# Performance work log

Hardware: AMD Instinct MI355X
Metric: run time of the kernel (lower is better)

## Reference

```python
import jax, jax.numpy as jnp
import numpy as np

HIDDEN = 2048
HEADS = 32
HEAD_DIM = HIDDEN // HEADS  # 64
MAX_POS = 512
TABLE = 2 * MAX_POS - 1  # 1023


def setup_inputs() -> dict:
    key = jax.random.key(0)
    k = jax.random.split(key, 6)
    B, S = 16, 512
    return {
        "hidden_states": jax.random.normal(k[0], (B, S, HIDDEN), dtype=jnp.float32),
        "wq": jax.random.normal(k[1], (HIDDEN, HIDDEN), dtype=jnp.float32) * 0.02,
        "wk": jax.random.normal(k[2], (HIDDEN, HIDDEN), dtype=jnp.float32) * 0.02,
        "wv": jax.random.normal(k[3], (HIDDEN, HIDDEN), dtype=jnp.float32) * 0.02,
        "wo": jax.random.normal(k[4], (HIDDEN, HIDDEN), dtype=jnp.float32) * 0.02,
        "rel_pos": jax.random.normal(k[5], (TABLE, HEAD_DIM), dtype=jnp.float32),
    }


def _rel_bias(rel_pos, seq_len):
    pos = jnp.arange(seq_len)
    rel = pos[None, :] - pos[:, None] + (MAX_POS - 1)  # [S, S]
    rel = jnp.clip(rel, 0, TABLE - 1)
    return rel_pos[rel].mean(axis=-1)  # [S, S]


def reference(hidden_states, wq, wk, wv, wo, rel_pos):
    B, S, _ = hidden_states.shape
    scale = jnp.sqrt(jnp.float32(HEAD_DIM))
    # nn.Linear(x) = x @ W.T
    q = (hidden_states @ wq.T).reshape(B, S, HEADS, HEAD_DIM).transpose(0, 2, 1, 3)
    k = (hidden_states @ wk.T).reshape(B, S, HEADS, HEAD_DIM).transpose(0, 2, 1, 3)
    v = (hidden_states @ wv.T).reshape(B, S, HEADS, HEAD_DIM).transpose(0, 2, 1, 3)
    scores = jnp.einsum("bhqd,bhkd->bhqk", q, k) / scale
    scores = scores + _rel_bias(rel_pos, S)[None, None]  # seq_len <= 512 path
    attn = jax.nn.softmax(scores, axis=-1)
    ctx = jnp.einsum("bhqk,bhkd->bhqd", attn, v)
    ctx = ctx.transpose(0, 2, 1, 3).reshape(B, S, HIDDEN)
    return ctx @ wo.T
```

## Files before the change

### kernel.cpp

```cpp
#include <hip/hip_runtime.h>

typedef __attribute__((ext_vector_type(8))) short bf16x8;
typedef __attribute__((ext_vector_type(4))) float f32x4;
typedef const __attribute__((address_space(3))) unsigned short* lds_cp;

#define DEVI __device__ __forceinline__

template <int N> struct IC { static constexpr int v = N; };

DEVI unsigned short f2bf(float f) {
  union { float f; unsigned u; } v; v.f = f;
  unsigned r = v.u + 0x7FFFu + ((v.u >> 16) & 1u);
  return (unsigned short)(r >> 16);
}

DEVI void gload16(const void* g, void* l) {
  __builtin_amdgcn_global_load_lds(
      (const __attribute__((address_space(1))) unsigned int*)g,
      (__attribute__((address_space(3))) unsigned int*)l, 16, 0, 0);
}

template <int OFF>
DEVI bf16x8 lreadT(lds_cp p) {
  bf16x8 r;
  asm volatile("ds_read_b128 %0, %1 offset:%2" : "=v"(r) : "v"(p), "i"(OFF));
  return r;
}

template <int OFF>
DEVI void read_af(lds_cp a0, lds_cp a1, bf16x8 (&f)[4][2]) {
  f[0][0] = lreadT<OFF + 0>(a0);    f[0][1] = lreadT<OFF + 0>(a1);
  f[1][0] = lreadT<OFF + 2048>(a0); f[1][1] = lreadT<OFF + 2048>(a1);
  f[2][0] = lreadT<OFF + 4096>(a0); f[2][1] = lreadT<OFF + 4096>(a1);
  f[3][0] = lreadT<OFF + 6144>(a0); f[3][1] = lreadT<OFF + 6144>(a1);
}
template <int OFF>
DEVI void read_bq(lds_cp b0, lds_cp b1, bf16x8 (&f)[2][2]) {
  f[0][0] = lreadT<OFF + 0>(b0);    f[0][1] = lreadT<OFF + 0>(b1);
  f[1][0] = lreadT<OFF + 2048>(b0); f[1][1] = lreadT<OFF + 2048>(b1);
}

#define MFMA16(a, b, c) __builtin_amdgcn_mfma_f32_16x16x32_bf16(a, b, c, 0, 0, 0)
#define LGKM(n) asm volatile("s_waitcnt lgkmcnt(" #n ")")
#define SBAR() __builtin_amdgcn_sched_barrier(0)

__global__ void prep_kernel(const float* __restrict__ x,
                            const float* __restrict__ wq,
                            const float* __restrict__ wk,
                            const float* __restrict__ wv,
                            const float* __restrict__ wo,
                            const float* __restrict__ rel,
                            unsigned short* __restrict__ xb,
                            unsigned short* __restrict__ wqb,
                            float* __restrict__ bias1) {
  const int blk = blockIdx.x;
  if (blk < 16384) {
    const int i = blk * 256 + threadIdx.x;
    float4 v = ((const float4*)x)[i];
    ushort4 o;
    o.x = f2bf(v.x); o.y = f2bf(v.y); o.z = f2bf(v.z); o.w = f2bf(v.w);
    ((ushort4*)xb)[i] = o;
  } else if (blk < 32768) {
    const int i = (blk - 16384) * 256 + threadIdx.x;
    const int w = i >> 20, l = i & 1048575;
    const float* s = (w == 0) ? wq : (w == 1) ? wk : (w == 2) ? wv : wo;
    float4 v = ((const float4*)s)[l];
    ushort4 o;
    o.x = f2bf(v.x); o.y = f2bf(v.y); o.z = f2bf(v.z); o.w = f2bf(v.w);
    ((ushort4*)wqb)[i] = o;
  } else {
    const int t = (blk - 32768) * 256 + threadIdx.x;
    if (t < 1023) {
      const float* r = rel + t * 64;
      float s = 0.f;
#pragma unroll
      for (int d = 0; d < 64; ++d) s += r[d];
      bias1[t] = s * (1.44269504f / 64.0f);
    }
  }
}

template <int MODE, int NT>
__global__ __launch_bounds__(512, 2) void gemm256(
    const unsigned short* __restrict__ A, const unsigned short* __restrict__ B,
    void* __restrict__ Cout, void* __restrict__ Cout2, void* __restrict__ Cout3) {
  __shared__ unsigned short As[2][16384];
  __shared__ unsigned short Bs[2][16384];

  const int tid = threadIdx.x;
  const int logical = (blockIdx.x & 7) * (4 * NT) + (blockIdx.x >> 3);
  const int nt = logical % NT, mt = logical / NT;
  const int m0 = mt * 256, n0 = nt * 256;
  const int lane = tid & 63, wid = tid >> 6;
  const int wr = wid >> 2, wc = wid & 3;
  const int g = lane >> 4, c = lane & 15;

  const int srow = tid >> 3, sj = (tid & 7) ^ (srow & 7);
  const unsigned short* pA0[2];
  const unsigned short* pB0[2];
  unsigned short* lA0[2];
  unsigned short* lB0[2];
#pragma unroll
  for (int ch = 0; ch < 2; ++ch) {
    const int row = ch * 64 + srow;
    pA0[ch] = A + (size_t)(m0 + row) * 2048u + sj * 8;
    pB0[ch] = B + (size_t)(n0 + row) * 2048u + sj * 8;
    const int slot = ch * 512 + tid;
    lA0[ch] = &As[0][slot * 8];
    lB0[ch] = &Bs[0][slot * 8];
  }

  const int rA = wr * 128 + c;
  const int rB = wc * 64 + c;
  lds_cp aA0 = (lds_cp)&As[0][rA * 64 + (((0 + g) ^ (rA & 7)) * 8)];
  lds_cp aA1 = (lds_cp)&As[0][rA * 64 + (((4 + g) ^ (rA & 7)) * 8)];
  lds_cp aB0 = (lds_cp)&Bs[0][rB * 64 + (((0 + g) ^ (rB & 7)) * 8)];
  lds_cp aB1 = (lds_cp)&Bs[0][rB * 64 + (((4 + g) ^ (rB & 7)) * 8)];

  f32x4 acc[8][4];
#pragma unroll
  for (int i = 0; i < 8; ++i)
#pragma unroll
    for (int j = 0; j < 4; ++j) acc[i][j] = (f32x4){0.f, 0.f, 0.f, 0.f};

  bf16x8 afl[4][2], afh[4][2], bq0[2][2], bq1[2][2];

#pragma unroll
  for (int ch = 0; ch < 2; ++ch) {
    gload16(pA0[ch], lA0[ch]);
    gload16(pA0[ch] + 262144, lA0[ch] + 8192);
    gload16(pB0[ch], lB0[ch]);
    gload16(pB0[ch] + 262144, lB0[ch] + 8192);
  }
#pragma unroll
  for (int ch = 0; ch < 2; ++ch) {
    gload16(pA0[ch] + 64, lA0[ch] + 16384);
    gload16(pA0[ch] + 262144 + 64, lA0[ch] + 8192 + 16384);
  }
  asm volatile("s_waitcnt vmcnt(4)" ::: "memory");
  SBAR();
  __builtin_amdgcn_s_barrier();

  auto ktile = [&](auto B_, auto SB_, auto SA_, auto LB_, auto LA_, int kt) {
    constexpr int BOFF = decltype(B_)::v;
    constexpr int SB = decltype(SB_)::v;
    constexpr int SA = decltype(SA_)::v;
    constexpr int LB = decltype(LB_)::v;
    constexpr int LA = decltype(LA_)::v;

    read_bq<BOFF>(aB0, aB1, bq0);
    read_af<BOFF>(aA0, aA1, afl);
    read_bq<BOFF + 4096>(aB0, aB1, bq1);
    read_af<BOFF + 8192>(aA0, aA1, afh);
    if (kt + 1 < 32) {
      gload16(pB0[0] + SB, lB0[0] + LB);
      gload16(pB0[1] + SB, lB0[1] + LB);
      gload16(pB0[0] + 262144 + SB, lB0[0] + 8192 + LB);
      gload16(pB0[1] + 262144 + SB, lB0[1] + 8192 + LB);
    }

    LGKM(12);
    SBAR();
    __builtin_amdgcn_s_setprio(1);
#pragma unroll
    for (int kk = 0; kk < 2; ++kk)
#pragma unroll
      for (int mi = 0; mi < 4; ++mi)
#pragma unroll
        for (int ni = 0; ni < 2; ++ni)
          acc[mi][ni] = MFMA16(afl[mi][kk], bq0[ni][kk], acc[mi][ni]);
    __builtin_amdgcn_s_setprio(0);

    LGKM(8);
    SBAR();
    __builtin_amdgcn_s_setprio(1);
#pragma unroll
    for (int kk = 0; kk < 2; ++kk)
#pragma unroll
      for (int mi = 0; mi < 4; ++mi)
#pragma unroll
        for (int ni = 0; ni < 2; ++ni)
          acc[mi][ni + 2] = MFMA16(afl[mi][kk], bq1[ni][kk], acc[mi][ni + 2]);
    __builtin_amdgcn_s_setprio(0);

    LGKM(0);
    SBAR();
    __builtin_amdgcn_s_barrier();
    if (kt + 2 < 32) {
      gload16(pA0[0] + SA, lA0[0] + LA);
      gload16(pA0[1] + SA, lA0[1] + LA);
      gload16(pA0[0] + 262144 + SA, lA0[0] + 8192 + LA);
      gload16(pA0[1] + 262144 + SA, lA0[1] + 8192 + LA);
    }

    __builtin_amdgcn_s_setprio(1);
#pragma unroll
    for (int kk = 0; kk < 2; ++kk)
#pragma unroll
      for (int mi = 0; mi < 4; ++mi)
#pragma unroll
        for (int ni = 0; ni < 2; ++ni)
          acc[mi + 4][ni] = MFMA16(afh[mi][kk], bq0[ni][kk], acc[mi + 4][ni]);
#pragma unroll
    for (int kk = 0; kk < 2; ++kk)
#pragma unroll
      for (int mi = 0; mi < 4; ++mi)
#pragma unroll
        for (int ni = 0; ni < 2; ++ni)
          acc[mi + 4][ni + 2] = MFMA16(afh[mi][kk], bq1[ni][kk], acc[mi + 4][ni + 2]);
    __builtin_amdgcn_s_setprio(0);

    if (kt < 30) {
      asm volatile("s_waitcnt vmcnt(4)" ::: "memory");
    } else {
      asm volatile("s_waitcnt vmcnt(0)" ::: "memory");
    }
    SBAR();
    __builtin_amdgcn_s_barrier();
  };

  for (int t2 = 0; t2 < 16; ++t2) {
    ktile(IC<0>{}, IC<64>{}, IC<128>{}, IC<16384>{}, IC<0>{}, 2 * t2);
    ktile(IC<32768>{}, IC<128>{}, IC<192>{}, IC<0>{}, IC<16384>{}, 2 * t2 + 1);
#pragma unroll
    for (int ch = 0; ch < 2; ++ch) { pA0[ch] += 128; pB0[ch] += 128; }
  }

  const int rbase = m0 + wr * 128 + g * 4;
  const int cbase = n0 + wc * 64 + c;
  if (MODE == 0) {
    float* O = (float*)Cout;
#pragma unroll
    for (int mi = 0; mi < 8; ++mi)
#pragma unroll
      for (int ni = 0; ni < 4; ++ni)
#pragma unroll
        for (int rr = 0; rr < 4; ++rr)
          O[(size_t)(rbase + mi * 16 + rr) * 2048u + (cbase + ni * 16)] =
              acc[mi][ni][rr];
  } else {
    const int qsel = cbase >> 11;
    if (qsel < 2) {
      unsigned short* O = (unsigned short*)(qsel == 0 ? Cout : Cout2);
#pragma unroll
      for (int mi = 0; mi < 8; ++mi)
#pragma unroll
        for (int ni = 0; ni < 4; ++ni)
#pragma unroll
          for (int rr = 0; rr < 4; ++rr)
            O[(size_t)(rbase + mi * 16 + rr) * 2048u +
              ((cbase + ni * 16) & 2047)] = f2bf(acc[mi][ni][rr]);
    } else {
      unsigned short* O = (unsigned short*)Cout3;
#pragma unroll
      for (int mi = 0; mi < 8; ++mi)
#pragma unroll
        for (int ni = 0; ni < 4; ++ni) {
          const int row = rbase + mi * 16;
          const int col = (cbase + ni * 16) & 2047;
          const int bq_ = row >> 9, s = row & 511;
          const int hh = col >> 6, dd = col & 63;
          ushort4 o;
          o.x = f2bf(acc[mi][ni][0]);
          o.y = f2bf(acc[mi][ni][1]);
          o.z = f2bf(acc[mi][ni][2]);
          o.w = f2bf(acc[mi][ni][3]);
          *(ushort4*)(O + ((size_t)((bq_ * 32 + hh) * 64 + dd) << 9) + s) = o;
        }
    }
  }
}

__global__ __launch_bounds__(256, 3) void attn_kernel(
    const unsigned short* __restrict__ Q, const unsigned short* __restrict__ K,
    const unsigned short* __restrict__ VT, const float* __restrict__ bias1d,
    unsigned short* __restrict__ CTX) {
  __shared__ unsigned short Ksh[2][4096];
  __shared__ unsigned short Vsh[2][4096];
  __shared__ unsigned short Pb[4][2048];
  __shared__ float bl[1024];

  const int tid = threadIdx.x;
  const int wave = tid >> 6;
  const int lane = tid & 63;
  const int g = lane >> 4, c = lane & 15;

  const int logical = (blockIdx.x & 7) * 256 + (blockIdx.x >> 3);
  const int qc = logical & 3;
  const int bh = logical >> 2;
  const int b = bh >> 5, h = bh & 31;
  const int qrow0 = qc * 128 + wave * 32;

  for (int i = tid; i < 1023; i += 256) bl[i] = bias1d[i];

  bf16x8 aq[2][2];
  {
    const unsigned short* qb =
        Q + (size_t)(b * 512 + qrow0 + c) * 2048u + h * 64 + g * 8;
#pragma unroll
    for (int mi = 0; mi < 2; ++mi)
#pragma unroll
      for (int kk = 0; kk < 2; ++kk)
        aq[mi][kk] = *(const bf16x8*)(qb + mi * 16 * 2048 + kk * 32);
  }

  const unsigned short* kgb = K + (size_t)(b * 512) * 2048u + h * 64;
  const unsigned short* vgb = VT + (size_t)(bh * 64) * 512u;

  auto stage = [&](int buf, int kt) {
#pragma unroll
    for (int half = 0; half < 2; ++half) {
      const int slot = half * 256 + wave * 64 + lane;
      const int row = slot >> 3;
      const int j = (slot & 7) ^ (row & 7);
      gload16(kgb + (size_t)(kt * 64 + row) * 2048u + j * 8,
              &Ksh[buf][slot * 8]);
      gload16(vgb + (size_t)row * 512u + kt * 64 + j * 8, &Vsh[buf][slot * 8]);
    }
  };

  f32x4 o[2][4];
#pragma unroll
  for (int mi = 0; mi < 2; ++mi)
#pragma unroll
    for (int di = 0; di < 4; ++di) o[mi][di] = (f32x4){0.f, 0.f, 0.f, 0.f};
  float lreg[2][4];
#pragma unroll
  for (int mi = 0; mi < 2; ++mi)
#pragma unroll
    for (int rr = 0; rr < 4; ++rr) lreg[mi][rr] = 0.f;

  stage(0, 0);
  __syncthreads();

  const float SSCALE = 0.125f * 1.44269504f;

  for (int kt = 0; kt < 8; ++kt) {
    const int buf = kt & 1;
    if (kt < 7) stage(buf ^ 1, kt + 1);

    f32x4 s[2][4];
#pragma unroll
    for (int ni = 0; ni < 4; ++ni) {
      const unsigned short* kr = &Ksh[buf][(ni * 16 + c) * 64];
      bf16x8 bk0 = *(const bf16x8*)(kr + ((0 + g) ^ (c & 7)) * 8);
      bf16x8 bk1 = *(const bf16x8*)(kr + ((4 + g) ^ (c & 7)) * 8);
#pragma unroll
      for (int mi = 0; mi < 2; ++mi) {
        f32x4 z = (f32x4){0.f, 0.f, 0.f, 0.f};
        z = MFMA16(aq[mi][0], bk0, z);
        z = MFMA16(aq[mi][1], bk1, z);
        s[mi][ni] = z;
      }
    }

    unsigned short* pw = &Pb[wave][0];
#pragma unroll
    for (int mi = 0; mi < 2; ++mi)
#pragma unroll
      for (int rr = 0; rr < 4; ++rr) {
        const int prow = mi * 16 + g * 4 + rr;
        const int off0 = kt * 64 + c - (qrow0 + prow) + 511;
        float e0 = __builtin_amdgcn_exp2f(s[mi][0][rr] * SSCALE + bl[off0]);
        float e1 = __builtin_amdgcn_exp2f(s[mi][1][rr] * SSCALE + bl[off0 + 16]);
        float e2 = __builtin_amdgcn_exp2f(s[mi][2][rr] * SSCALE + bl[off0 + 32]);
        float e3 = __builtin_amdgcn_exp2f(s[mi][3][rr] * SSCALE + bl[off0 + 48]);
        lreg[mi][rr] += (e0 + e1) + (e2 + e3);
        const int rx = prow * 64, sw = (c >> 3) ^ (prow & 7), cl = c & 7;
        pw[rx + ((0 ^ sw) * 8 | cl)] = f2bf(e0);
        pw[rx + ((2 ^ sw) * 8 | cl)] = f2bf(e1);
        pw[rx + ((4 ^ sw) * 8 | cl)] = f2bf(e2);
        pw[rx + ((6 ^ sw) * 8 | cl)] = f2bf(e3);
      }

#pragma unroll
    for (int kk = 0; kk < 2; ++kk) {
      bf16x8 pa0 =
          *(const bf16x8*)(pw + (0 + c) * 64 + ((kk * 4 + g) ^ (c & 7)) * 8);
      bf16x8 pa1 =
          *(const bf16x8*)(pw + (16 + c) * 64 + ((kk * 4 + g) ^ (c & 7)) * 8);
#pragma unroll
      for (int di = 0; di < 4; ++di) {
        bf16x8 vb = *(const bf16x8*)(&Vsh[buf][(di * 16 + c) * 64 +
                                               ((kk * 4 + g) ^ (c & 7)) * 8]);
        o[0][di] = MFMA16(pa0, vb, o[0][di]);
        o[1][di] = MFMA16(pa1, vb, o[1][di]);
      }
    }
    __syncthreads();
  }

#pragma unroll
  for (int mi = 0; mi < 2; ++mi)
#pragma unroll
    for (int rr = 0; rr < 4; ++rr) {
      float l = lreg[mi][rr];
      l += __shfl_xor(l, 1);
      l += __shfl_xor(l, 2);
      l += __shfl_xor(l, 4);
      l += __shfl_xor(l, 8);
      const float rl = __builtin_amdgcn_rcpf(l);
      unsigned short* ob =
          CTX + (size_t)(b * 512 + qrow0 + mi * 16 + g * 4 + rr) * 2048u +
          h * 64 + c;
#pragma unroll
      for (int di = 0; di < 4; ++di) ob[di * 16] = f2bf(o[mi][di][rr] * rl);
    }
}

extern "C" void kernel_launch(void* const* d_in, const int* in_sizes, int n_in,
                              void* d_out, int out_size, void* d_ws,
                              size_t ws_size, hipStream_t stream) {
  const float* x = (const float*)d_in[0];
  const float* wq = (const float*)d_in[1];
  const float* wk = (const float*)d_in[2];
  const float* wv = (const float*)d_in[3];
  const float* wo = (const float*)d_in[4];
  const float* rel = (const float*)d_in[5];

  char* ws = (char*)d_ws;
  unsigned short* xb = (unsigned short*)(ws);
  unsigned short* wqb = (unsigned short*)(ws + 33554432);
  unsigned short* wob = wqb + 3 * 4194304;
  unsigned short* qb = (unsigned short*)(ws + 67108864);
  unsigned short* kb = qb + 16777216;
  unsigned short* vt = kb + 16777216;
  float* bias1 = (float*)(ws + 167772160);
  unsigned short* ctx = xb;

  prep_kernel<<<32772, 256, 0, stream>>>(x, wq, wk, wv, wo, rel, xb, wqb,
                                         bias1);

  gemm256<3, 24><<<768, 512, 0, stream>>>(xb, wqb, qb, kb, vt);

  attn_kernel<<<2048, 256, 0, stream>>>(qb, kb, vt, bias1, ctx);

  gemm256<0, 8><<<256, 512, 0, stream>>>(ctx, wob, (float*)d_out, nullptr,
                                         nullptr);
}
```

Baseline: 334.0 us.

## Load K/V fragments directly from global in attention, drop LDS staging

Removes the double-buffered LDS staging of K and V tiles in the attention kernel. Each wave now reads its MFMA B-operands straight from global memory (relying on L1/L2 for reuse across the four waves) and no longer synchronises per tile. Freeing LDS allows the launch bound to rise to four blocks per CU, and s_setprio wraps the MFMA sections. The trade is redundant global/cache traffic across waves and exposed load latency, since there is no prefetch.

Result: slower. 411.9 us (+23.3%).

```diff
diff --git a/kernel.cpp b/kernel.cpp
--- a/kernel.cpp
+++ b/kernel.cpp
@@ -271,12 +271,10 @@
   }
 }
 
-__global__ __launch_bounds__(256, 3) void attn_kernel(
+__global__ __launch_bounds__(256, 4) void attn_kernel(
     const unsigned short* __restrict__ Q, const unsigned short* __restrict__ K,
     const unsigned short* __restrict__ VT, const float* __restrict__ bias1d,
     unsigned short* __restrict__ CTX) {
-  __shared__ unsigned short Ksh[2][4096];
-  __shared__ unsigned short Vsh[2][4096];
   __shared__ unsigned short Pb[4][2048];
   __shared__ float bl[1024];
 
@@ -303,21 +301,11 @@
       for (int kk = 0; kk < 2; ++kk)
         aq[mi][kk] = *(const bf16x8*)(qb + mi * 16 * 2048 + kk * 32);
   }
-
-  const unsigned short* kgb = K + (size_t)(b * 512) * 2048u + h * 64;
-  const unsigned short* vgb = VT + (size_t)(bh * 64) * 512u;
-
-  auto stage = [&](int buf, int kt) {
-#pragma unroll
-    for (int half = 0; half < 2; ++half) {
-      const int slot = half * 256 + wave * 64 + lane;
-      const int row = slot >> 3;
-      const int j = (slot & 7) ^ (row & 7);
-      gload16(kgb + (size_t)(kt * 64 + row) * 2048u + j * 8,
-              &Ksh[buf][slot * 8]);
-      gload16(vgb + (size_t)row * 512u + kt * 64 + j * 8, &Vsh[buf][slot * 8]);
-    }
-  };
+  __syncthreads();
+
+  const unsigned short* kgb =
+      K + (size_t)(b * 512) * 2048u + h * 64 + g * 8;
+  const unsigned short* vgb = VT + (size_t)(bh * 64) * 512u + g * 8;
 
   f32x4 o[2][4];
 #pragma unroll
@@ -330,21 +318,16 @@
 #pragma unroll
     for (int rr = 0; rr < 4; ++rr) lreg[mi][rr] = 0.f;
 
-  stage(0, 0);
-  __syncthreads();
-
   const float SSCALE = 0.125f * 1.44269504f;
 
   for (int kt = 0; kt < 8; ++kt) {
-    const int buf = kt & 1;
-    if (kt < 7) stage(buf ^ 1, kt + 1);
-
     f32x4 s[2][4];
+    __builtin_amdgcn_s_setprio(1);
 #pragma unroll
     for (int ni = 0; ni < 4; ++ni) {
-      const unsigned short* kr = &Ksh[buf][(ni * 16 + c) * 64];
-      bf16x8 bk0 = *(const bf16x8*)(kr + ((0 + g) ^ (c & 7)) * 8);
-      bf16x8 bk1 = *(const bf16x8*)(kr + ((4 + g) ^ (c & 7)) * 8);
+      const unsigned short* kr = kgb + (size_t)(kt * 64 + ni * 16 + c) * 2048u;
+      bf16x8 bk0 = *(const bf16x8*)(kr);
+      bf16x8 bk1 = *(const bf16x8*)(kr + 32);
 #pragma unroll
       for (int mi = 0; mi < 2; ++mi) {
         f32x4 z = (f32x4){0.f, 0.f, 0.f, 0.f};
@@ -353,6 +336,7 @@
         s[mi][ni] = z;
       }
     }
+    __builtin_amdgcn_s_setprio(0);
 
     unsigned short* pw = &Pb[wave][0];
 #pragma unroll
@@ -373,6 +357,7 @@
         pw[rx + ((6 ^ sw) * 8 | cl)] = f2bf(e3);
       }
 
+    __builtin_amdgcn_s_setprio(1);
 #pragma unroll
     for (int kk = 0; kk < 2; ++kk) {
       bf16x8 pa0 =
@@ -381,13 +366,13 @@
           *(const bf16x8*)(pw + (16 + c) * 64 + ((kk * 4 + g) ^ (c & 7)) * 8);
 #pragma unroll
       for (int di = 0; di < 4; ++di) {
-        bf16x8 vb = *(const bf16x8*)(&Vsh[buf][(di * 16 + c) * 64 +
-                                               ((kk * 4 + g) ^ (c & 7)) * 8]);
+        bf16x8 vb = *(const bf16x8*)(vgb + (size_t)(di * 16 + c) * 512u +
+                                     kt * 64 + kk * 32);
         o[0][di] = MFMA16(pa0, vb, o[0][di]);
         o[1][di] = MFMA16(pa1, vb, o[1][di]);
       }
     }
-    __syncthreads();
+    __builtin_amdgcn_s_setprio(0);
   }
 
 #pragma unroll
```

## Switch GEMM inner loop to 32x32x16 MFMA with k-step register pipelining

Applied to the files above, without the earlier changes.

Replaces the 16x16x32 bf16 MFMA tiling in the 256x256 GEMM with 32x32x16 MFMAs. Each wave now holds 4x2 32x32 accumulators, and LDS fragment reads are reorganized into four k-slices that are double-buffered in registers, so ds_reads for the next slice overlap the current MFMA cluster. The larger MFMA shape cuts the number of LDS fragment reads per FLOP and the instruction count. In exchange it changes the LDS read pattern and swizzle use, and the epilogue index mapping had to be rewritten to match.

Result: slower. 361.5 us (+8.3%).

```diff
diff --git a/kernel.cpp b/kernel.cpp
--- a/kernel.cpp
+++ b/kernel.cpp
@@ -2,6 +2,7 @@
 
 typedef __attribute__((ext_vector_type(8))) short bf16x8;
 typedef __attribute__((ext_vector_type(4))) float f32x4;
+typedef __attribute__((ext_vector_type(16))) float f32x16;
 typedef const __attribute__((address_space(3))) unsigned short* lds_cp;
 
 #define DEVI __device__ __forceinline__
@@ -27,20 +28,8 @@
   return r;
 }
 
-template <int OFF>
-DEVI void read_af(lds_cp a0, lds_cp a1, bf16x8 (&f)[4][2]) {
-  f[0][0] = lreadT<OFF + 0>(a0);    f[0][1] = lreadT<OFF + 0>(a1);
-  f[1][0] = lreadT<OFF + 2048>(a0); f[1][1] = lreadT<OFF + 2048>(a1);
-  f[2][0] = lreadT<OFF + 4096>(a0); f[2][1] = lreadT<OFF + 4096>(a1);
-  f[3][0] = lreadT<OFF + 6144>(a0); f[3][1] = lreadT<OFF + 6144>(a1);
-}
-template <int OFF>
-DEVI void read_bq(lds_cp b0, lds_cp b1, bf16x8 (&f)[2][2]) {
-  f[0][0] = lreadT<OFF + 0>(b0);    f[0][1] = lreadT<OFF + 0>(b1);
-  f[1][0] = lreadT<OFF + 2048>(b0); f[1][1] = lreadT<OFF + 2048>(b1);
-}
-
 #define MFMA16(a, b, c) __builtin_amdgcn_mfma_f32_16x16x32_bf16(a, b, c, 0, 0, 0)
+#define MFMA32(a, b, c) __builtin_amdgcn_mfma_f32_32x32x16_bf16(a, b, c, 0, 0, 0)
 #define LGKM(n) asm volatile("s_waitcnt lgkmcnt(" #n ")")
 #define SBAR() __builtin_amdgcn_sched_barrier(0)
 
@@ -93,7 +82,7 @@
   const int m0 = mt * 256, n0 = nt * 256;
   const int lane = tid & 63, wid = tid >> 6;
   const int wr = wid >> 2, wc = wid & 3;
-  const int g = lane >> 4, c = lane & 15;
+  const int ln31 = lane & 31, h = lane >> 5;
 
   const int srow = tid >> 3, sj = (tid & 7) ^ (srow & 7);
   const unsigned short* pA0[2];
@@ -110,20 +99,26 @@
     lB0[ch] = &Bs[0][slot * 8];
   }
 
-  const int rA = wr * 128 + c;
-  const int rB = wc * 64 + c;
-  lds_cp aA0 = (lds_cp)&As[0][rA * 64 + (((0 + g) ^ (rA & 7)) * 8)];
-  lds_cp aA1 = (lds_cp)&As[0][rA * 64 + (((4 + g) ^ (rA & 7)) * 8)];
-  lds_cp aB0 = (lds_cp)&Bs[0][rB * 64 + (((0 + g) ^ (rB & 7)) * 8)];
-  lds_cp aB1 = (lds_cp)&Bs[0][rB * 64 + (((4 + g) ^ (rB & 7)) * 8)];
-
-  f32x4 acc[8][4];
-#pragma unroll
-  for (int i = 0; i < 8; ++i)
-#pragma unroll
-    for (int j = 0; j < 4; ++j) acc[i][j] = (f32x4){0.f, 0.f, 0.f, 0.f};
-
-  bf16x8 afl[4][2], afh[4][2], bq0[2][2], bq1[2][2];
+  const int rowA = wr * 128 + ln31;
+  const int rowB = wc * 64 + ln31;
+  const int x7 = ln31 & 7;
+  lds_cp aAk[4], aBk[4];
+#pragma unroll
+  for (int kk = 0; kk < 4; ++kk) {
+    const int slot = ((kk * 2 + h) ^ x7) * 8;
+    aAk[kk] = (lds_cp)&As[0][rowA * 64 + slot];
+    aBk[kk] = (lds_cp)&Bs[0][rowB * 64 + slot];
+  }
+
+  f32x16 acc[4][2];
+#pragma unroll
+  for (int i = 0; i < 4; ++i)
+#pragma unroll
+    for (int j = 0; j < 2; ++j)
+#pragma unroll
+      for (int e = 0; e < 16; ++e) acc[i][j][e] = 0.f;
+
+  bf16x8 a[2][4], b[2][2];
 
 #pragma unroll
   for (int ch = 0; ch < 2; ++ch) {
@@ -140,6 +135,28 @@
   asm volatile("s_waitcnt vmcnt(4)" ::: "memory");
   SBAR();
   __builtin_amdgcn_s_barrier();
+
+  auto issueG = [&](auto P_, auto KK_, auto B_) {
+    constexpr int P = decltype(P_)::v;
+    constexpr int KK = decltype(KK_)::v;
+    constexpr int BOFF = decltype(B_)::v;
+    b[P][0] = lreadT<BOFF + 0>(aBk[KK]);
+    b[P][1] = lreadT<BOFF + 4096>(aBk[KK]);
+    a[P][0] = lreadT<BOFF + 0>(aAk[KK]);
+    a[P][1] = lreadT<BOFF + 4096>(aAk[KK]);
+    a[P][2] = lreadT<BOFF + 8192>(aAk[KK]);
+    a[P][3] = lreadT<BOFF + 12288>(aAk[KK]);
+  };
+  auto cluster = [&](auto P_) {
+    constexpr int P = decltype(P_)::v;
+    __builtin_amdgcn_s_setprio(1);
+#pragma unroll
+    for (int fi = 0; fi < 4; ++fi)
+#pragma unroll
+      for (int fj = 0; fj < 2; ++fj)
+        acc[fi][fj] = MFMA32(a[P][fi], b[P][fj], acc[fi][fj]);
+    __builtin_amdgcn_s_setprio(0);
+  };
 
   auto ktile = [&](auto B_, auto SB_, auto SA_, auto LB_, auto LA_, int kt) {
     constexpr int BOFF = decltype(B_)::v;
@@ -148,10 +165,8 @@
     constexpr int LB = decltype(LB_)::v;
     constexpr int LA = decltype(LA_)::v;
 
-    read_bq<BOFF>(aB0, aB1, bq0);
-    read_af<BOFF>(aA0, aA1, afl);
-    read_bq<BOFF + 4096>(aB0, aB1, bq1);
-    read_af<BOFF + 8192>(aA0, aA1, afh);
+    issueG(IC<0>{}, IC<0>{}, IC<BOFF>{});
+    issueG(IC<1>{}, IC<1>{}, IC<BOFF>{});
     if (kt + 1 < 32) {
       gload16(pB0[0] + SB, lB0[0] + LB);
       gload16(pB0[1] + SB, lB0[1] + LB);
@@ -159,29 +174,19 @@
       gload16(pB0[1] + 262144 + SB, lB0[1] + 8192 + LB);
     }
 
-    LGKM(12);
+    LGKM(6);
     SBAR();
-    __builtin_amdgcn_s_setprio(1);
-#pragma unroll
-    for (int kk = 0; kk < 2; ++kk)
-#pragma unroll
-      for (int mi = 0; mi < 4; ++mi)
-#pragma unroll
-        for (int ni = 0; ni < 2; ++ni)
-          acc[mi][ni] = MFMA16(afl[mi][kk], bq0[ni][kk], acc[mi][ni]);
-    __builtin_amdgcn_s_setprio(0);
-
-    LGKM(8);
+    cluster(IC<0>{});
+    issueG(IC<0>{}, IC<2>{}, IC<BOFF>{});
+
+    LGKM(6);
     SBAR();
-    __builtin_amdgcn_s_setprio(1);
-#pragma unroll
-    for (int kk = 0; kk < 2; ++kk)
-#pragma unroll
-      for (int mi = 0; mi < 4; ++mi)
-#pragma unroll
-        for (int ni = 0; ni < 2; ++ni)
-          acc[mi][ni + 2] = MFMA16(afl[mi][kk], bq1[ni][kk], acc[mi][ni + 2]);
-    __builtin_amdgcn_s_setprio(0);
+    cluster(IC<1>{});
+    issueG(IC<1>{}, IC<3>{}, IC<BOFF>{});
+
+    LGKM(6);
+    SBAR();
+    cluster(IC<0>{});
 
     LGKM(0);
     SBAR();
@@ -192,23 +197,7 @@
       gload16(pA0[0] + 262144 + SA, lA0[0] + 8192 + LA);
       gload16(pA0[1] + 262144 + SA, lA0[1] + 8192 + LA);
     }
-
-    __builtin_amdgcn_s_setprio(1);
-#pragma unroll
-    for (int kk = 0; kk < 2; ++kk)
-#pragma unroll
-      for (int mi = 0; mi < 4; ++mi)
-#pragma unroll
-        for (int ni = 0; ni < 2; ++ni)
-          acc[mi + 4][ni] = MFMA16(afh[mi][kk], bq0[ni][kk], acc[mi + 4][ni]);
-#pragma unroll
-    for (int kk = 0; kk < 2; ++kk)
-#pragma unroll
-      for (int mi = 0; mi < 4; ++mi)
-#pragma unroll
-        for (int ni = 0; ni < 2; ++ni)
-          acc[mi + 4][ni + 2] = MFMA16(afh[mi][kk], bq1[ni][kk], acc[mi + 4][ni + 2]);
-    __builtin_amdgcn_s_setprio(0);
+    cluster(IC<1>{});
 
     if (kt < 30) {
       asm volatile("s_waitcnt vmcnt(4)" ::: "memory");
@@ -226,47 +215,53 @@
     for (int ch = 0; ch < 2; ++ch) { pA0[ch] += 128; pB0[ch] += 128; }
   }
 
-  const int rbase = m0 + wr * 128 + g * 4;
-  const int cbase = n0 + wc * 64 + c;
+  const int rowbase = m0 + wr * 128 + 4 * h;
+  const int colbase = n0 + wc * 64 + ln31;
   if (MODE == 0) {
     float* O = (float*)Cout;
 #pragma unroll
-    for (int mi = 0; mi < 8; ++mi)
-#pragma unroll
-      for (int ni = 0; ni < 4; ++ni)
-#pragma unroll
-        for (int rr = 0; rr < 4; ++rr)
-          O[(size_t)(rbase + mi * 16 + rr) * 2048u + (cbase + ni * 16)] =
-              acc[mi][ni][rr];
+    for (int fi = 0; fi < 4; ++fi)
+#pragma unroll
+      for (int fj = 0; fj < 2; ++fj)
+#pragma unroll
+        for (int q = 0; q < 4; ++q)
+#pragma unroll
+          for (int j = 0; j < 4; ++j)
+            O[(size_t)(rowbase + fi * 32 + 8 * q + j) * 2048u +
+              (colbase + fj * 32)] = acc[fi][fj][4 * q + j];
   } else {
-    const int qsel = cbase >> 11;
+    const int qsel = n0 >> 11;
     if (qsel < 2) {
       unsigned short* O = (unsigned short*)(qsel == 0 ? Cout : Cout2);
 #pragma unroll
-      for (int mi = 0; mi < 8; ++mi)
-#pragma unroll
-        for (int ni = 0; ni < 4; ++ni)
-#pragma unroll
-          for (int rr = 0; rr < 4; ++rr)
-            O[(size_t)(rbase + mi * 16 + rr) * 2048u +
-              ((cbase + ni * 16) & 2047)] = f2bf(acc[mi][ni][rr]);
+      for (int fi = 0; fi < 4; ++fi)
+#pragma unroll
+        for (int fj = 0; fj < 2; ++fj)
+#pragma unroll
+          for (int q = 0; q < 4; ++q)
+#pragma unroll
+            for (int j = 0; j < 4; ++j)
+              O[(size_t)(rowbase + fi * 32 + 8 * q + j) * 2048u +
+                ((colbase + fj * 32) & 2047)] = f2bf(acc[fi][fj][4 * q + j]);
     } else {
       unsigned short* O = (unsigned short*)Cout3;
 #pragma unroll
-      for (int mi = 0; mi < 8; ++mi)
-#pragma unroll
-        for (int ni = 0; ni < 4; ++ni) {
-          const int row = rbase + mi * 16;
-          const int col = (cbase + ni * 16) & 2047;
-          const int bq_ = row >> 9, s = row & 511;
-          const int hh = col >> 6, dd = col & 63;
-          ushort4 o;
-          o.x = f2bf(acc[mi][ni][0]);
-          o.y = f2bf(acc[mi][ni][1]);
-          o.z = f2bf(acc[mi][ni][2]);
-          o.w = f2bf(acc[mi][ni][3]);
-          *(ushort4*)(O + ((size_t)((bq_ * 32 + hh) * 64 + dd) << 9) + s) = o;
-        }
+      for (int fi = 0; fi < 4; ++fi)
+#pragma unroll
+        for (int fj = 0; fj < 2; ++fj)
+#pragma unroll
+          for (int q = 0; q < 4; ++q) {
+            const int row = rowbase + fi * 32 + 8 * q;
+            const int col = (colbase + fj * 32) & 2047;
+            const int bq_ = row >> 9, s = row & 511;
+            const int hh = col >> 6, dd = col & 63;
+            ushort4 o;
+            o.x = f2bf(acc[fi][fj][4 * q + 0]);
+            o.y = f2bf(acc[fi][fj][4 * q + 1]);
+            o.z = f2bf(acc[fi][fj][4 * q + 2]);
+            o.w = f2bf(acc[fi][fj][4 * q + 3]);
+            *(ushort4*)(O + ((size_t)((bq_ * 32 + hh) * 64 + dd) << 9) + s) = o;
+          }
     }
   }
 }
```
